# Performance work log

Measured on AMD Instinct MI355X. Metric: run time of the kernel, lower is better.

The kernel has to match this reference:

```python
import jax, jax.numpy as jnp
import numpy as np

VOCAB = 4101
NUM_IGNORED = 5  # token ids {0,1,2,3,4} are ignored


def _calc_frequency(x):
    # x: [N, L] int token ids -> [N, VOCAB] scaled frequency vectors
    n = x.shape[0]
    hist = jnp.zeros((n, VOCAB), dtype=jnp.float32)
    hist = hist.at[jnp.arange(n)[:, None], x].add(1.0)  # batched bincount
    hist = hist.at[:, :NUM_IGNORED].set(0.0)            # drop ignored tokens
    seq_len = hist.sum(axis=-1, keepdims=True)          # count of kept tokens
    return jnp.where(seq_len > 0, hist / seq_len * 10.0, hist)


def _mlp(h, W1, b1, W2, b2):
    h = jax.nn.relu(h @ W1 + b1)
    return h @ W2 + b2


def setup_inputs() -> dict:
    key = jax.random.key(0)
    k1, k2, k3 = jax.random.split(key, 3)
    B, L = 1024, 4096
    X = jax.random.randint(k1, (B, 3, L), 0, VOCAB, dtype=jnp.int64)
    W1 = jax.random.normal(k2, (VOCAB, 768), dtype=jnp.float32) * 0.02
    b1 = jnp.zeros((768,), dtype=jnp.float32)
    W2 = jax.random.normal(k3, (768, 256), dtype=jnp.float32) * 0.02
    b2 = jnp.zeros((256,), dtype=jnp.float32)
    return {"X": X, "W1": W1, "b1": b1, "W2": W2, "b2": b2}


def reference(X, W1, b1, W2, b2):
    B, three, L = X.shape
    flat = X.reshape(B * three, L)          # process anchor/pos/neg together
    freq = _calc_frequency(flat)            # [3B, VOCAB]
    out = _mlp(freq, W1, b1, W2, b2)        # [3B, 256]
    out = out.reshape(B, three, 256)
    return (out[:, 0], out[:, 1], out[:, 2])
```

## Files before the change

### kernel.cpp

```cpp
#include <hip/hip_runtime.h>

typedef unsigned short ushort_t;
typedef __bf16 bf16_8 __attribute__((ext_vector_type(8)));
typedef float f32x4 __attribute__((ext_vector_type(4)));

#define VOCAB 4101
#define KPAD  4224
#define NROWS 3072
#define HDIM  768
#define ODIM  256


static __device__ __forceinline__ unsigned short f2bf(float f) {
  unsigned int u = __float_as_uint(f);
  unsigned int r = (u + 0x7fffu + ((u >> 16) & 1u)) >> 16;
  return (unsigned short)r;
}

static __device__ __forceinline__ void async_copy16(const void* g, void* l) {
  __builtin_amdgcn_global_load_lds(
      (const __attribute__((address_space(1))) void*)g,
      (__attribute__((address_space(3))) void*)l, 16, 0, 0);
}


__global__ __launch_bounds__(256)
void hist_kernel(const int* __restrict__ X, ushort_t* __restrict__ A,
                 float* __restrict__ scales) {
  const int r = blockIdx.x;
  __shared__ unsigned int h[KPAD];
  for (int i = threadIdx.x; i < KPAD; i += 256) h[i] = 0u;
  __syncthreads();

  const int4* xp = reinterpret_cast<const int4*>(X + (size_t)r * 4096);
  #pragma unroll
  for (int i = 0; i < 4; ++i) {
    int4 v = xp[i * 256 + threadIdx.x];
    atomicAdd(&h[v.x], 1u);
    atomicAdd(&h[v.y], 1u);
    atomicAdd(&h[v.z], 1u);
    atomicAdd(&h[v.w], 1u);
  }
  __syncthreads();

  const unsigned int ignored = h[0] + h[1] + h[2] + h[3] + h[4];
  const float s = 10.0f / (float)(4096u - ignored);
  if (threadIdx.x == 0) scales[r] = s;

  unsigned int* Ar = (unsigned int*)(A + (size_t)r * KPAD);
  for (int i = threadIdx.x; i < KPAD / 2; i += 256) {
    int i0 = 2 * i, i1 = 2 * i + 1;
    unsigned int c0 = (i0 >= 5 && i0 < VOCAB) ? h[i0] : 0u;
    unsigned int c1 = (i1 >= 5 && i1 < VOCAB) ? h[i1] : 0u;
    Ar[i] = (unsigned int)f2bf((float)c0) | ((unsigned int)f2bf((float)c1) << 16);
  }
}


__global__ __launch_bounds__(256)
void transpose_convert(const float* __restrict__ src, ushort_t* __restrict__ dst,
                       int K, int N, int Kpad) {
  __shared__ ushort_t tile[64][65];
  const int kb = blockIdx.x * 64;
  const int nb = blockIdx.y * 64;
  const int tr = threadIdx.x >> 6;
  const int tc = threadIdx.x & 63;
  #pragma unroll
  for (int i = 0; i < 16; ++i) {
    int r = i * 4 + tr;
    int k = kb + r;
    float v = (k < K) ? src[(size_t)k * N + nb + tc] : 0.0f;
    tile[r][tc] = f2bf(v);
  }
  __syncthreads();
  #pragma unroll
  for (int i = 0; i < 16; ++i) {
    int r = i * 4 + tr;
    dst[(size_t)(nb + r) * Kpad + kb + tc] = tile[tc][r];
  }
}


__global__ __launch_bounds__(384)
void gemm1_fused(const ushort_t* __restrict__ A, int lda,
                 const ushort_t* __restrict__ Bt, int ldb,
                 int ktiles,
                 const float* __restrict__ scales,
                 const float* __restrict__ bias,
                 ushort_t* __restrict__ H) {
  __shared__ __align__(16) ushort_t Alds[2][96 * 128];
  __shared__ __align__(16) ushort_t Blds[2][96 * 128];
  const int tid  = threadIdx.x;
  const int lane = tid & 63;
  const int wv   = tid >> 6;
  const int wrow = wv / 3;
  const int wcol = wv % 3;
  const int m0   = blockIdx.x * 96;
  const int n0   = blockIdx.y * 96;

  f32x4 acc[3][2];
  #pragma unroll
  for (int m = 0; m < 3; ++m)
    #pragma unroll
    for (int n = 0; n < 2; ++n)
      acc[m][n] = (f32x4){0.f, 0.f, 0.f, 0.f};

#define STAGE(bi, kt)                                                          \
  {                                                                            \
    const int k0_ = (kt) * 128;                                                \
    _Pragma("unroll")                                                          \
    for (int i = 0; i < 4; ++i) {                                              \
      const int cd  = i * 384 + tid;                                           \
      const int row = cd >> 4;                                                 \
      const int cc  = (cd & 15) ^ (row & 7);                                   \
      async_copy16(A + (size_t)(m0 + row) * lda + k0_ + cc * 8,                \
                   (char*)&Alds[bi][0] + cd * 16);                             \
    }                                                                          \
    _Pragma("unroll")                                                          \
    for (int i = 0; i < 4; ++i) {                                              \
      const int cd  = i * 384 + tid;                                           \
      const int row = cd >> 4;                                                 \
      const int cc  = (cd & 15) ^ (row & 7);                                   \
      async_copy16(Bt + (size_t)(n0 + row) * ldb + k0_ + cc * 8,               \
                   (char*)&Blds[bi][0] + cd * 16);                             \
    }                                                                          \
  }

  STAGE(0, 0);
  __syncthreads();

  int cur = 0;
  for (int t = 0; t < ktiles; ++t) {
    if (t + 1 < ktiles) STAGE(cur ^ 1, t + 1);
    const int hi = lane >> 4;
    #pragma unroll
    for (int kk = 0; kk < 4; ++kk) {
      bf16_8 af[3], bf[2];
      #pragma unroll
      for (int m = 0; m < 3; ++m) {
        const int ra = wrow * 48 + m * 16 + (lane & 15);
        const int ca = kk * 4 + hi;
        af[m] = *(const bf16_8*)((const char*)&Alds[cur][0] +
                                 (ra * 16 + (ca ^ (ra & 7))) * 16);
      }
      #pragma unroll
      for (int n = 0; n < 2; ++n) {
        const int rb = wcol * 32 + n * 16 + (lane & 15);
        const int cb = kk * 4 + hi;
        bf[n] = *(const bf16_8*)((const char*)&Blds[cur][0] +
                                 (rb * 16 + (cb ^ (rb & 7))) * 16);
      }
      #pragma unroll
      for (int m = 0; m < 3; ++m)
        #pragma unroll
        for (int n = 0; n < 2; ++n)
          acc[m][n] = __builtin_amdgcn_mfma_f32_16x16x32_bf16(af[m], bf[n],
                                                              acc[m][n], 0, 0, 0);
    }
    __syncthreads();
    cur ^= 1;
  }
#undef STAGE

  const int rbase = (lane >> 4) * 4;
  const int cf    = lane & 15;
  #pragma unroll
  for (int m = 0; m < 3; ++m) {
    #pragma unroll
    for (int n = 0; n < 2; ++n) {
      #pragma unroll
      for (int reg = 0; reg < 4; ++reg) {
        const int gr = m0 + wrow * 48 + m * 16 + rbase + reg;
        const int gc = n0 + wcol * 32 + n * 16 + cf;
        float v = fmaxf(acc[m][n][reg] * scales[gr] + bias[gc], 0.0f);
        H[(size_t)gr * HDIM + gc] = f2bf(v);
      }
    }
  }
}


__global__ __launch_bounds__(384)
void gemm2_fused(const ushort_t* __restrict__ A, int lda,
                 const ushort_t* __restrict__ Bt, int ldb,
                 int ktiles,
                 const float* __restrict__ bias,
                 float* __restrict__ outp) {
  __shared__ __align__(16) ushort_t Alds[2][96 * 128];
  __shared__ __align__(16) ushort_t Blds[2][32 * 128];
  const int tid  = threadIdx.x;
  const int lane = tid & 63;
  const int wv   = tid >> 6;
  const int m0   = blockIdx.x * 96;
  const int n0   = blockIdx.y * 32;

  f32x4 acc[2];
  acc[0] = (f32x4){0.f, 0.f, 0.f, 0.f};
  acc[1] = (f32x4){0.f, 0.f, 0.f, 0.f};

#define STAGE(bi, kt)                                                          \
  {                                                                            \
    const int k0_ = (kt) * 128;                                                \
    _Pragma("unroll")                                                          \
    for (int i = 0; i < 4; ++i) {                                              \
      const int cd  = i * 384 + tid;                                           \
      const int row = cd >> 4;                                                 \
      const int cc  = (cd & 15) ^ (row & 7);                                   \
      async_copy16(A + (size_t)(m0 + row) * lda + k0_ + cc * 8,                \
                   (char*)&Alds[bi][0] + cd * 16);                             \
    }                                                                          \
    {                                                                          \
      const int cd  = tid;                                                     \
      const int row = cd >> 4;                                                 \
      const int cc  = (cd & 15) ^ (row & 7);                                   \
      async_copy16(Bt + (size_t)(n0 + row) * ldb + k0_ + cc * 8,               \
                   (char*)&Blds[bi][0] + cd * 16);                             \
    }                                                                          \
    if (tid < 128) {                                                           \
      const int cd  = 384 + tid;                                               \
      const int row = cd >> 4;                                                 \
      const int cc  = (cd & 15) ^ (row & 7);                                   \
      async_copy16(Bt + (size_t)(n0 + row) * ldb + k0_ + cc * 8,               \
                   (char*)&Blds[bi][0] + cd * 16);                             \
    }                                                                          \
  }

  STAGE(0, 0);
  __syncthreads();

  int cur = 0;
  for (int t = 0; t < ktiles; ++t) {
    if (t + 1 < ktiles) STAGE(cur ^ 1, t + 1);
    const int hi = lane >> 4;
    #pragma unroll
    for (int kk = 0; kk < 4; ++kk) {
      bf16_8 af, bf[2];
      {
        const int ra = wv * 16 + (lane & 15);
        const int ca = kk * 4 + hi;
        af = *(const bf16_8*)((const char*)&Alds[cur][0] +
                              (ra * 16 + (ca ^ (ra & 7))) * 16);
      }
      #pragma unroll
      for (int n = 0; n < 2; ++n) {
        const int rb = n * 16 + (lane & 15);
        const int cb = kk * 4 + hi;
        bf[n] = *(const bf16_8*)((const char*)&Blds[cur][0] +
                                 (rb * 16 + (cb ^ (rb & 7))) * 16);
      }
      #pragma unroll
      for (int n = 0; n < 2; ++n)
        acc[n] = __builtin_amdgcn_mfma_f32_16x16x32_bf16(af, bf[n], acc[n], 0, 0, 0);
    }
    __syncthreads();
    cur ^= 1;
  }
#undef STAGE

  const int rbase = (lane >> 4) * 4;
  const int cf    = lane & 15;
  #pragma unroll
  for (int n = 0; n < 2; ++n) {
    #pragma unroll
    for (int reg = 0; reg < 4; ++reg) {
      const int gr = m0 + wv * 16 + rbase + reg;
      const int gc = n0 + n * 16 + cf;
      float v = acc[n][reg] + bias[gc];
      outp[(size_t)(gr % 3) * (1024 * ODIM) + (size_t)(gr / 3) * ODIM + gc] = v;
    }
  }
}


extern "C" void kernel_launch(void* const* d_in, const int* in_sizes, int n_in,
                              void* d_out, int out_size, void* d_ws, size_t ws_size,
                              hipStream_t stream) {
  const int*   X  = (const int*)d_in[0];
  const float* W1 = (const float*)d_in[1];
  const float* b1 = (const float*)d_in[2];
  const float* W2 = (const float*)d_in[3];
  const float* b2 = (const float*)d_in[4];
  float* out = (float*)d_out;

  char* ws = (char*)d_ws;
  ushort_t* A      = (ushort_t*)(ws);
  ushort_t* W1T    = (ushort_t*)(ws + 25952256);
  ushort_t* H      = (ushort_t*)(ws + 32440320);
  ushort_t* W2T    = (ushort_t*)(ws + 37158912);
  float*    scales = (float*)   (ws + 37552128);

  hist_kernel<<<NROWS, 256, 0, stream>>>(X, A, scales);
  transpose_convert<<<dim3(KPAD / 64, HDIM / 64), 256, 0, stream>>>(W1, W1T, VOCAB, HDIM, KPAD);
  transpose_convert<<<dim3(HDIM / 64, ODIM / 64), 256, 0, stream>>>(W2, W2T, HDIM, ODIM, HDIM);

  gemm1_fused<<<dim3(NROWS / 96, HDIM / 96), 384, 0, stream>>>(
      A, KPAD, W1T, KPAD, KPAD / 128, scales, b1, H);

  gemm2_fused<<<dim3(NROWS / 96, ODIM / 32), 384, 0, stream>>>(
      H, HDIM, W2T, HDIM, HDIM / 128, b2, out);
}
```

Before: 72.01 us.

## Merge histogram and weight transposes into one launch; retile gemm1 to four waves

The histogram kernel and the two weight transpose/convert kernels are folded into a single prep kernel that picks its role from the block index. This removes two kernel launches and lets the transpose blocks overlap with the histogram blocks. Separately, gemm1 now runs 256 threads, with each of four waves computing a 48x48 sub-tile (3x3 MFMAs) instead of six waves computing 48x32. That gives each wave more MFMA work per LDS fragment load, but it uses more accumulator registers and has fewer waves available to hide latency.

```diff
diff --git a/kernel.cpp b/kernel.cpp
--- a/kernel.cpp
+++ b/kernel.cpp
@@ -25,63 +25,77 @@
 
 
 __global__ __launch_bounds__(256)
-void hist_kernel(const int* __restrict__ X, ushort_t* __restrict__ A,
+void prep_kernel(const int* __restrict__ X,
+                 const float* __restrict__ W1,
+                 const float* __restrict__ W2,
+                 ushort_t* __restrict__ A,
+                 ushort_t* __restrict__ W1T,
+                 ushort_t* __restrict__ W2T,
                  float* __restrict__ scales) {
-  const int r = blockIdx.x;
-  __shared__ unsigned int h[KPAD];
-  for (int i = threadIdx.x; i < KPAD; i += 256) h[i] = 0u;
-  __syncthreads();
-
-  const int4* xp = reinterpret_cast<const int4*>(X + (size_t)r * 4096);
-  #pragma unroll
-  for (int i = 0; i < 4; ++i) {
-    int4 v = xp[i * 256 + threadIdx.x];
-    atomicAdd(&h[v.x], 1u);
-    atomicAdd(&h[v.y], 1u);
-    atomicAdd(&h[v.z], 1u);
-    atomicAdd(&h[v.w], 1u);
-  }
-  __syncthreads();
-
-  const unsigned int ignored = h[0] + h[1] + h[2] + h[3] + h[4];
-  const float s = 10.0f / (float)(4096u - ignored);
-  if (threadIdx.x == 0) scales[r] = s;
-
-  unsigned int* Ar = (unsigned int*)(A + (size_t)r * KPAD);
-  for (int i = threadIdx.x; i < KPAD / 2; i += 256) {
-    int i0 = 2 * i, i1 = 2 * i + 1;
-    unsigned int c0 = (i0 >= 5 && i0 < VOCAB) ? h[i0] : 0u;
-    unsigned int c1 = (i1 >= 5 && i1 < VOCAB) ? h[i1] : 0u;
-    Ar[i] = (unsigned int)f2bf((float)c0) | ((unsigned int)f2bf((float)c1) << 16);
+  __shared__ __align__(16) unsigned char smem[16896];
+  const int bid = blockIdx.x;
+
+  if (bid < NROWS) {
+    unsigned int* h = (unsigned int*)smem;
+    const int r = bid;
+    for (int i = threadIdx.x; i < KPAD; i += 256) h[i] = 0u;
+    __syncthreads();
+
+    const int4* xp = reinterpret_cast<const int4*>(X + (size_t)r * 4096);
+    #pragma unroll
+    for (int i = 0; i < 4; ++i) {
+      int4 v = xp[i * 256 + threadIdx.x];
+      atomicAdd(&h[v.x], 1u);
+      atomicAdd(&h[v.y], 1u);
+      atomicAdd(&h[v.z], 1u);
+      atomicAdd(&h[v.w], 1u);
+    }
+    __syncthreads();
+
+    const unsigned int ignored = h[0] + h[1] + h[2] + h[3] + h[4];
+    const float s = 10.0f / (float)(4096u - ignored);
+    if (threadIdx.x == 0) scales[r] = s;
+
+    unsigned int* Ar = (unsigned int*)(A + (size_t)r * KPAD);
+    for (int i = threadIdx.x; i < KPAD / 2; i += 256) {
+      int i0 = 2 * i, i1 = 2 * i + 1;
+      unsigned int c0 = (i0 >= 5 && i0 < VOCAB) ? h[i0] : 0u;
+      unsigned int c1 = (i1 >= 5 && i1 < VOCAB) ? h[i1] : 0u;
+      Ar[i] = (unsigned int)f2bf((float)c0) | ((unsigned int)f2bf((float)c1) << 16);
+    }
+  } else {
+    ushort_t (*tile)[65] = (ushort_t(*)[65])smem;
+    const float* src; ushort_t* dst;
+    int K, N, Kpad, kb, nb;
+    if (bid < NROWS + 792) {
+      const int t = bid - NROWS;
+      src = W1; dst = W1T; K = VOCAB; N = HDIM; Kpad = KPAD;
+      kb = (t % 66) * 64; nb = (t / 66) * 64;
+    } else {
+      const int t = bid - NROWS - 792;
+      src = W2; dst = W2T; K = HDIM; N = ODIM; Kpad = HDIM;
+      kb = (t % 12) * 64; nb = (t / 12) * 64;
+    }
+    const int tr = threadIdx.x >> 6;
+    const int tc = threadIdx.x & 63;
+    #pragma unroll
+    for (int i = 0; i < 16; ++i) {
+      int r = i * 4 + tr;
+      int k = kb + r;
+      float v = (k < K) ? src[(size_t)k * N + nb + tc] : 0.0f;
+      tile[r][tc] = f2bf(v);
+    }
+    __syncthreads();
+    #pragma unroll
+    for (int i = 0; i < 16; ++i) {
+      int r = i * 4 + tr;
+      dst[(size_t)(nb + r) * Kpad + kb + tc] = tile[tc][r];
+    }
   }
 }
 
 
 __global__ __launch_bounds__(256)
-void transpose_convert(const float* __restrict__ src, ushort_t* __restrict__ dst,
-                       int K, int N, int Kpad) {
-  __shared__ ushort_t tile[64][65];
-  const int kb = blockIdx.x * 64;
-  const int nb = blockIdx.y * 64;
-  const int tr = threadIdx.x >> 6;
-  const int tc = threadIdx.x & 63;
-  #pragma unroll
-  for (int i = 0; i < 16; ++i) {
-    int r = i * 4 + tr;
-    int k = kb + r;
-    float v = (k < K) ? src[(size_t)k * N + nb + tc] : 0.0f;
-    tile[r][tc] = f2bf(v);
-  }
-  __syncthreads();
-  #pragma unroll
-  for (int i = 0; i < 16; ++i) {
-    int r = i * 4 + tr;
-    dst[(size_t)(nb + r) * Kpad + kb + tc] = tile[tc][r];
-  }
-}
-
-
-__global__ __launch_bounds__(384)
 void gemm1_fused(const ushort_t* __restrict__ A, int lda,
                  const ushort_t* __restrict__ Bt, int ldb,
                  int ktiles,
@@ -93,32 +107,32 @@
   const int tid  = threadIdx.x;
   const int lane = tid & 63;
   const int wv   = tid >> 6;
-  const int wrow = wv / 3;
-  const int wcol = wv % 3;
+  const int wrow = wv >> 1;
+  const int wcol = wv & 1;
   const int m0   = blockIdx.x * 96;
   const int n0   = blockIdx.y * 96;
 
-  f32x4 acc[3][2];
+  f32x4 acc[3][3];
   #pragma unroll
   for (int m = 0; m < 3; ++m)
     #pragma unroll
-    for (int n = 0; n < 2; ++n)
+    for (int n = 0; n < 3; ++n)
       acc[m][n] = (f32x4){0.f, 0.f, 0.f, 0.f};
 
 #define STAGE(bi, kt)                                                          \
   {                                                                            \
     const int k0_ = (kt) * 128;                                                \
     _Pragma("unroll")                                                          \
-    for (int i = 0; i < 4; ++i) {                                              \
-      const int cd  = i * 384 + tid;                                           \
+    for (int i = 0; i < 6; ++i) {                                              \
+      const int cd  = i * 256 + tid;                                           \
       const int row = cd >> 4;                                                 \
       const int cc  = (cd & 15) ^ (row & 7);                                   \
       async_copy16(A + (size_t)(m0 + row) * lda + k0_ + cc * 8,                \
                    (char*)&Alds[bi][0] + cd * 16);                             \
     }                                                                          \
     _Pragma("unroll")                                                          \
-    for (int i = 0; i < 4; ++i) {                                              \
-      const int cd  = i * 384 + tid;                                           \
+    for (int i = 0; i < 6; ++i) {                                              \
+      const int cd  = i * 256 + tid;                                           \
       const int row = cd >> 4;                                                 \
       const int cc  = (cd & 15) ^ (row & 7);                                   \
       async_copy16(Bt + (size_t)(n0 + row) * ldb + k0_ + cc * 8,               \
@@ -135,7 +149,7 @@
     const int hi = lane >> 4;
     #pragma unroll
     for (int kk = 0; kk < 4; ++kk) {
-      bf16_8 af[3], bf[2];
+      bf16_8 af[3], bf[3];
       #pragma unroll
       for (int m = 0; m < 3; ++m) {
         const int ra = wrow * 48 + m * 16 + (lane & 15);
@@ -144,8 +158,8 @@
                                  (ra * 16 + (ca ^ (ra & 7))) * 16);
       }
       #pragma unroll
-      for (int n = 0; n < 2; ++n) {
-        const int rb = wcol * 32 + n * 16 + (lane & 15);
+      for (int n = 0; n < 3; ++n) {
+        const int rb = wcol * 48 + n * 16 + (lane & 15);
         const int cb = kk * 4 + hi;
         bf[n] = *(const bf16_8*)((const char*)&Blds[cur][0] +
                                  (rb * 16 + (cb ^ (rb & 7))) * 16);
@@ -153,7 +167,7 @@
       #pragma unroll
       for (int m = 0; m < 3; ++m)
         #pragma unroll
-        for (int n = 0; n < 2; ++n)
+        for (int n = 0; n < 3; ++n)
           acc[m][n] = __builtin_amdgcn_mfma_f32_16x16x32_bf16(af[m], bf[n],
                                                               acc[m][n], 0, 0, 0);
     }
@@ -167,11 +181,11 @@
   #pragma unroll
   for (int m = 0; m < 3; ++m) {
     #pragma unroll
-    for (int n = 0; n < 2; ++n) {
+    for (int n = 0; n < 3; ++n) {
       #pragma unroll
       for (int reg = 0; reg < 4; ++reg) {
         const int gr = m0 + wrow * 48 + m * 16 + rbase + reg;
-        const int gc = n0 + wcol * 32 + n * 16 + cf;
+        const int gc = n0 + wcol * 48 + n * 16 + cf;
         float v = fmaxf(acc[m][n][reg] * scales[gr] + bias[gc], 0.0f);
         H[(size_t)gr * HDIM + gc] = f2bf(v);
       }
@@ -289,11 +303,9 @@
   ushort_t* W2T    = (ushort_t*)(ws + 37158912);
   float*    scales = (float*)   (ws + 37552128);
 
-  hist_kernel<<<NROWS, 256, 0, stream>>>(X, A, scales);
-  transpose_convert<<<dim3(KPAD / 64, HDIM / 64), 256, 0, stream>>>(W1, W1T, VOCAB, HDIM, KPAD);
-  transpose_convert<<<dim3(HDIM / 64, ODIM / 64), 256, 0, stream>>>(W2, W2T, HDIM, ODIM, HDIM);
-
-  gemm1_fused<<<dim3(NROWS / 96, HDIM / 96), 384, 0, stream>>>(
+  prep_kernel<<<NROWS + 792 + 48, 256, 0, stream>>>(X, W1, W2, A, W1T, W2T, scales);
+
+  gemm1_fused<<<dim3(NROWS / 96, HDIM / 96), 256, 0, stream>>>(
       A, KPAD, W1T, KPAD, KPAD / 128, scales, b1, H);
 
   gemm2_fused<<<dim3(NROWS / 96, ODIM / 32), 384, 0, stream>>>(
```

Measured after the change: 63.16 us, median of 2. 12.3% less time.
